# Kernel tuning notes

Hardware: AMD Instinct MI355X
Metric: run time of the kernel (lower is better)

## Reference

```python
import jax, jax.numpy as jnp
import numpy as np

B, T, E = 2, 2048, 1024
H = 16
D = E // H  # 64

def setup_inputs() -> dict:
    key = jax.random.key(0)
    kx, kq, kk, kv, ko = jax.random.split(key, 5)
    s = 1.0 / np.sqrt(E)
    return {
        "x":  jax.random.normal(kx, (B, T, E), dtype=jnp.float32),
        "Wq": jax.random.normal(kq, (E, E), dtype=jnp.float32) * s,
        "Wk": jax.random.normal(kk, (E, E), dtype=jnp.float32) * s,
        "Wv": jax.random.normal(kv, (E, E), dtype=jnp.float32) * s,
        "Wo": jax.random.normal(ko, (E, E), dtype=jnp.float32) * s,
    }

def reference(x, Wq, Wk, Wv, Wo):
    # Faithful to the torch module, including its quirks:
    #  - head split is a raw .view(B, H, T, D) reshape (NOT a transpose split)
    #  - masked_fill result is discarded in the original, so NO causal mask is applied
    #  - dropout = 0.0 -> identity
    b, t, e = x.shape
    q = jnp.reshape(x @ Wq, (b, H, t, D))
    k = jnp.reshape(x @ Wk, (b, H, t, D))
    v = jnp.reshape(x @ Wv, (b, H, t, D))
    # raw_score = q @ k^T ; softmax over keys of raw_score / sqrt(head_dim)
    scores = jnp.einsum("bhtd,bhsd->bhts", q, k) / jnp.sqrt(jnp.asarray(D, x.dtype))
    attn = jax.nn.softmax(scores, axis=-1)
    h = jnp.einsum("bhts,bhsd->bhtd", attn, v)           # (B,H,T,D)
    h = jnp.reshape(h, (b, t, e))                         # .view(B, T, -1)
    return h @ Wo
```

## Files before the change

kernel.cpp:

```cpp
#include <hip/hip_runtime.h>
#include <hip/hip_bf16.h>
#include <math.h>

#define BB 2
#define TT 2048
#define EE 1024
#define HH 16
#define DD 64
#define MM (BB*TT)

typedef __bf16 bf16;
typedef bf16 bf16x8 __attribute__((ext_vector_type(8)));
typedef bf16 bf16x4 __attribute__((ext_vector_type(4)));
typedef float f32x4 __attribute__((ext_vector_type(4)));

#define MFMA16(a,b,c) __builtin_amdgcn_mfma_f32_16x16x32_bf16((a),(b),(c),0,0,0)

__device__ __forceinline__ void gload_lds16(const void* g, void* l) {
  __builtin_amdgcn_global_load_lds(
      (const __attribute__((address_space(1))) unsigned int*)g,
      (__attribute__((address_space(3))) unsigned int*)l, 16, 0, 0);
}

__device__ __forceinline__ unsigned short bits(bf16 h) {
  return __builtin_bit_cast(unsigned short, h);
}

__global__ __launch_bounds__(256) void prep(const float* __restrict__ x,
                                            const float* __restrict__ w0,
                                            const float* __restrict__ w1,
                                            const float* __restrict__ w2,
                                            const float* __restrict__ w3,
                                            bf16* __restrict__ xb,
                                            bf16* t0, bf16* t1, bf16* t2, bf16* t3) {
  __shared__ bf16 tile[64][65];
  const int bid = blockIdx.x;
  if (bid < 4096) {
    const int i = bid * 256 + threadIdx.x;
    float4 f = ((const float4*)x)[i];
    bf16x4 h;
    h[0] = (bf16)f.x; h[1] = (bf16)f.y; h[2] = (bf16)f.z; h[3] = (bf16)f.w;
    ((bf16x4*)xb)[i] = h;
    return;
  }
  const int t = bid - 4096;
  const int z = t >> 8, rem = t & 255;
  const float* W = z == 0 ? w0 : z == 1 ? w1 : z == 2 ? w2 : w3;
  bf16* T = z == 0 ? t0 : z == 1 ? t1 : z == 2 ? t2 : t3;
  const int n0 = (rem & 15) * 64, k0 = (rem >> 4) * 64;
#pragma unroll
  for (int i = 0; i < 16; i++) {
    int idx = threadIdx.x + i * 256;
    int r = idx >> 6, c = idx & 63;
    tile[c][r] = (bf16)W[(size_t)(k0 + r) * EE + n0 + c];
  }
  __syncthreads();
#pragma unroll
  for (int i = 0; i < 16; i++) {
    int idx = threadIdx.x + i * 256;
    int r = idx >> 6, c = idx & 63;
    T[(size_t)(n0 + r) * EE + k0 + c] = tile[r][c];
  }
}

template <typename OutT>
__device__ __forceinline__ void gemm_core(const bf16* __restrict__ A, const bf16* __restrict__ Bt,
                                          OutT* __restrict__ C, bf16* As, bf16* Bs) {
  const int tid = threadIdx.x;
  const int w = tid >> 6, lane = tid & 63;
  const int lg = lane >> 4, lr = lane & 15;
  const int row0 = blockIdx.y * 128, col0 = blockIdx.x * 128;
  const int wrow = (w >> 1) * 64, wcol = (w & 1) * 64;
  f32x4 acc[4][4];
#pragma unroll
  for (int m = 0; m < 4; m++)
#pragma unroll
    for (int n = 0; n < 4; n++) acc[m][n] = f32x4{0.f, 0.f, 0.f, 0.f};

  for (int kt = 0; kt < EE; kt += 32) {
#pragma unroll
    for (int i = 0; i < 2; i++) {
      const int c = i * 4 + w;
      const int row = c * 16 + (lane >> 2);
      const int kof = (lane & 3) * 8;
      gload_lds16(A + (size_t)(row0 + row) * EE + kt + kof, &As[c * 512]);
      gload_lds16(Bt + (size_t)(col0 + row) * EE + kt + kof, &Bs[c * 512]);
    }
    __syncthreads();
    bf16x8 a[4], b[4];
#pragma unroll
    for (int m = 0; m < 4; m++)
      a[m] = *(const bf16x8*)&As[(wrow + m * 16 + lr) * 32 + lg * 8];
#pragma unroll
    for (int n = 0; n < 4; n++)
      b[n] = *(const bf16x8*)&Bs[(wcol + n * 16 + lr) * 32 + lg * 8];
#pragma unroll
    for (int m = 0; m < 4; m++)
#pragma unroll
      for (int n = 0; n < 4; n++) acc[m][n] = MFMA16(a[m], b[n], acc[m][n]);
    __syncthreads();
  }
#pragma unroll
  for (int m = 0; m < 4; m++)
#pragma unroll
    for (int n = 0; n < 4; n++)
#pragma unroll
      for (int r = 0; r < 4; r++) {
        const int rr = row0 + wrow + m * 16 + lg * 4 + r;
        const int cc = col0 + wcol + n * 16 + lr;
        C[(size_t)rr * EE + cc] = (OutT)acc[m][n][r];
      }
}

__global__ __launch_bounds__(256) void gemm_qkv(const bf16* __restrict__ A,
                                                const bf16* __restrict__ w0,
                                                const bf16* __restrict__ w1,
                                                const bf16* __restrict__ w2,
                                                bf16* o0, bf16* o1, bf16* o2) {
  __shared__ __align__(16) bf16 As[128 * 32];
  __shared__ __align__(16) bf16 Bs[128 * 32];
  const bf16* Bt = (blockIdx.z == 0) ? w0 : (blockIdx.z == 1) ? w1 : w2;
  bf16* C = (blockIdx.z == 0) ? o0 : (blockIdx.z == 1) ? o1 : o2;
  gemm_core<bf16>(A, Bt, C, As, Bs);
}

__global__ __launch_bounds__(256) void gemm_out(const bf16* __restrict__ A,
                                                const bf16* __restrict__ Bt,
                                                float* __restrict__ C) {
  __shared__ __align__(16) bf16 As[128 * 32];
  __shared__ __align__(16) bf16 Bs[64 * 32];
  const int tid = threadIdx.x;
  const int w = tid >> 6, lane = tid & 63;
  const int lg = lane >> 4, lr = lane & 15;
  const int row0 = blockIdx.y * 128, col0 = blockIdx.x * 64;
  const int wrow = (w >> 1) * 64, wcol = (w & 1) * 32;
  f32x4 acc[4][2];
#pragma unroll
  for (int m = 0; m < 4; m++)
#pragma unroll
    for (int n = 0; n < 2; n++) acc[m][n] = f32x4{0.f, 0.f, 0.f, 0.f};

  for (int kt = 0; kt < EE; kt += 32) {
#pragma unroll
    for (int i = 0; i < 3; i++) {
      const int c = i * 4 + w;
      const int r16 = lane >> 2, kof = (lane & 3) * 8;
      if (c < 8)
        gload_lds16(A + (size_t)(row0 + c * 16 + r16) * EE + kt + kof, &As[c * 512]);
      else
        gload_lds16(Bt + (size_t)(col0 + (c - 8) * 16 + r16) * EE + kt + kof,
                    &Bs[(c - 8) * 512]);
    }
    __syncthreads();
    bf16x8 a[4], b[2];
#pragma unroll
    for (int m = 0; m < 4; m++)
      a[m] = *(const bf16x8*)&As[(wrow + m * 16 + lr) * 32 + lg * 8];
#pragma unroll
    for (int n = 0; n < 2; n++)
      b[n] = *(const bf16x8*)&Bs[(wcol + n * 16 + lr) * 32 + lg * 8];
#pragma unroll
    for (int m = 0; m < 4; m++)
#pragma unroll
      for (int n = 0; n < 2; n++) acc[m][n] = MFMA16(a[m], b[n], acc[m][n]);
    __syncthreads();
  }
#pragma unroll
  for (int m = 0; m < 4; m++)
#pragma unroll
    for (int n = 0; n < 2; n++)
#pragma unroll
      for (int r = 0; r < 4; r++) {
        const int rr = row0 + wrow + m * 16 + lg * 4 + r;
        const int cc = col0 + wcol + n * 16 + lr;
        C[(size_t)rr * EE + cc] = acc[m][n][r];
      }
}

__global__ __launch_bounds__(256, 2) void flash_attn(const bf16* __restrict__ Q,
                                                     const bf16* __restrict__ K,
                                                     const bf16* __restrict__ V,
                                                     bf16* __restrict__ Hout) {
  const int tid = threadIdx.x;
  const int w = tid >> 6, lane = tid & 63;
  const int hi = lane >> 4, lr = lane & 15;
  const int qh = w & 1, sh2 = w >> 1;

  const int bid = blockIdx.x + 16 * blockIdx.y;
  const int sid = (bid & 7) * 64 + (bid >> 3);
  const int qb = sid & 15, bh = sid >> 4;

  const size_t base = (size_t)(bh >> 4) * TT * EE + (size_t)(bh & 15) * 128 * EE;
  const bf16* qh_p = Q + base;
  const bf16* kh = K + base;
  const bf16* vh = V + base;
  bf16* hh = Hout + base;
  const int qbase = qb * 128 + qh * 64;

  __shared__ __align__(16) bf16 smem[4 * 64 * 72];
  bf16* KsBuf = smem;
  bf16* VtBuf = smem + 2 * 64 * 72;

  const float qscale = 0.18033688011112042f;
  bf16x8 aq[4][2];
#pragma unroll
  for (int rg = 0; rg < 4; rg++)
#pragma unroll
    for (int kk = 0; kk < 2; kk++) {
      bf16x8 qv = *(const bf16x8*)(qh_p + (size_t)(qbase + rg * 16 + lr) * DD + kk * 32 + hi * 8);
#pragma unroll
      for (int j = 0; j < 8; j++) qv[j] = (bf16)(qscale * (float)qv[j]);
      aq[rg][kk] = qv;
    }

  float l_[4] = {0.f, 0.f, 0.f, 0.f};
  f32x4 o[4][4];
#pragma unroll
  for (int rg = 0; rg < 4; rg++)
#pragma unroll
    for (int d = 0; d < 4; d++) o[rg][d] = f32x4{0.f, 0.f, 0.f, 0.f};

  const int krow = tid >> 2, kg8 = (tid & 3) * 8;
  const int vsp = tid & 31, vdb = (tid >> 5) * 4;
  const int s0p = 2 * vsp;
  const int vcs = (s0p & 32) | (((s0p >> 2) & 3) << 3) | (((s0p >> 4) & 1) << 2) | (s0p & 3);

  bf16x8 kr0 = *(const bf16x8*)(kh + (size_t)krow * DD + kg8);
  bf16x8 kr1 = *(const bf16x8*)(kh + (size_t)krow * DD + kg8 + 32);
  bf16x4 va0 = *(const bf16x4*)(vh + (size_t)(2 * vsp) * DD + vdb);
  bf16x4 vb0 = *(const bf16x4*)(vh + (size_t)(2 * vsp + 1) * DD + vdb);
  bf16x4 va1 = *(const bf16x4*)(vh + (size_t)(2 * vsp) * DD + vdb + 32);
  bf16x4 vb1 = *(const bf16x4*)(vh + (size_t)(2 * vsp + 1) * DD + vdb + 32);
  *(bf16x8*)&KsBuf[krow * 72 + kg8] = kr0;
  *(bf16x8*)&KsBuf[krow * 72 + kg8 + 32] = kr1;
#pragma unroll
  for (int j = 0; j < 4; j++) {
    unsigned u0 = (unsigned)bits(va0[j]) | ((unsigned)bits(vb0[j]) << 16);
    unsigned u1 = (unsigned)bits(va1[j]) | ((unsigned)bits(vb1[j]) << 16);
    *(unsigned*)&VtBuf[(vdb + j) * 72 + vcs] = u0;
    *(unsigned*)&VtBuf[(vdb + 32 + j) * 72 + vcs] = u1;
  }
  kr0 = *(const bf16x8*)(kh + (size_t)(64 + krow) * DD + kg8);
  kr1 = *(const bf16x8*)(kh + (size_t)(64 + krow) * DD + kg8 + 32);
  va0 = *(const bf16x4*)(vh + (size_t)(64 + 2 * vsp) * DD + vdb);
  vb0 = *(const bf16x4*)(vh + (size_t)(64 + 2 * vsp + 1) * DD + vdb);
  va1 = *(const bf16x4*)(vh + (size_t)(64 + 2 * vsp) * DD + vdb + 32);
  vb1 = *(const bf16x4*)(vh + (size_t)(64 + 2 * vsp + 1) * DD + vdb + 32);
  __syncthreads();

  for (int t = 0; t < TT / 64; t++) {
    const bf16* Kc = &KsBuf[(t & 1) * 64 * 72];
    const bf16* Vc = &VtBuf[(t & 1) * 64 * 72];

    f32x4 sA[4][2];
#pragma unroll
    for (int rg = 0; rg < 4; rg++)
#pragma unroll
      for (int cfl = 0; cfl < 2; cfl++) sA[rg][cfl] = f32x4{0.f, 0.f, 0.f, 0.f};
#pragma unroll
    for (int cfl = 0; cfl < 2; cfl++)
#pragma unroll
      for (int kk = 0; kk < 2; kk++) {
        bf16x8 bk = *(const bf16x8*)&Kc[(sh2 * 32 + cfl * 16 + lr) * 72 + kk * 32 + hi * 8];
#pragma unroll
        for (int rg = 0; rg < 4; rg++) sA[rg][cfl] = MFMA16(bk, aq[rg][kk], sA[rg][cfl]);
      }

    bf16x8 bp[4];
#pragma unroll
    for (int rg = 0; rg < 4; rg++) {
      f32x4 pr[2];
#pragma unroll
      for (int cfl = 0; cfl < 2; cfl++)
#pragma unroll
        for (int r = 0; r < 4; r++) {
          float p = __builtin_amdgcn_exp2f(sA[rg][cfl][r]);
          l_[rg] += p;
          pr[cfl][r] = p;
        }
#pragma unroll
      for (int j = 0; j < 8; j++) bp[rg][j] = (bf16)pr[j >> 2][j & 3];
    }

#pragma unroll
    for (int dblk = 0; dblk < 4; dblk++) {
      bf16x8 av = *(const bf16x8*)&Vc[(dblk * 16 + lr) * 72 + sh2 * 32 + hi * 8];
#pragma unroll
      for (int rg = 0; rg < 4; rg++) o[rg][dblk] = MFMA16(av, bp[rg], o[rg][dblk]);
    }

    if (t < TT / 64 - 1) {
      bf16* Kn = &KsBuf[((t + 1) & 1) * 64 * 72];
      bf16* Vn = &VtBuf[((t + 1) & 1) * 64 * 72];
      *(bf16x8*)&Kn[krow * 72 + kg8] = kr0;
      *(bf16x8*)&Kn[krow * 72 + kg8 + 32] = kr1;
#pragma unroll
      for (int j = 0; j < 4; j++) {
        unsigned u0 = (unsigned)bits(va0[j]) | ((unsigned)bits(vb0[j]) << 16);
        unsigned u1 = (unsigned)bits(va1[j]) | ((unsigned)bits(vb1[j]) << 16);
        *(unsigned*)&Vn[(vdb + j) * 72 + vcs] = u0;
        *(unsigned*)&Vn[(vdb + 32 + j) * 72 + vcs] = u1;
      }
      if (t < TT / 64 - 2) {
        const int s2 = (t + 2) * 64;
        kr0 = *(const bf16x8*)(kh + (size_t)(s2 + krow) * DD + kg8);
        kr1 = *(const bf16x8*)(kh + (size_t)(s2 + krow) * DD + kg8 + 32);
        va0 = *(const bf16x4*)(vh + (size_t)(s2 + 2 * vsp) * DD + vdb);
        vb0 = *(const bf16x4*)(vh + (size_t)(s2 + 2 * vsp + 1) * DD + vdb);
        va1 = *(const bf16x4*)(vh + (size_t)(s2 + 2 * vsp) * DD + vdb + 32);
        vb1 = *(const bf16x4*)(vh + (size_t)(s2 + 2 * vsp + 1) * DD + vdb + 32);
      }
    }
    __syncthreads();
  }

  float lt[4];
#pragma unroll
  for (int rg = 0; rg < 4; rg++) {
    lt[rg] = l_[rg];
    lt[rg] += __shfl_xor(lt[rg], 16);
    lt[rg] += __shfl_xor(lt[rg], 32);
  }
  float* sc = (float*)smem;
  float* scl = sc + 2 * 64 * 68;
  if (sh2 == 1) {
#pragma unroll
    for (int rg = 0; rg < 4; rg++) {
#pragma unroll
      for (int dblk = 0; dblk < 4; dblk++)
        *(f32x4*)&sc[qh * 4352 + (rg * 16 + lr) * 68 + dblk * 16 + 4 * hi] = o[rg][dblk];
      if (hi == 0) scl[qh * 64 + rg * 16 + lr] = lt[rg];
    }
  }
  __syncthreads();
  if (sh2 == 0) {
#pragma unroll
    for (int rg = 0; rg < 4; rg++) {
      const float ltot = lt[rg] + scl[qh * 64 + rg * 16 + lr];
      const float inv = 1.0f / ltot;
#pragma unroll
      for (int dblk = 0; dblk < 4; dblk++) {
        f32x4 ob = *(const f32x4*)&sc[qh * 4352 + (rg * 16 + lr) * 68 + dblk * 16 + 4 * hi];
        bf16x4 st;
#pragma unroll
        for (int r = 0; r < 4; r++) st[r] = (bf16)((o[rg][dblk][r] + ob[r]) * inv);
        *(bf16x4*)(hh + (size_t)(qbase + rg * 16 + lr) * DD + dblk * 16 + 4 * hi) = st;
      }
    }
  }
}

extern "C" void kernel_launch(void* const* d_in, const int* in_sizes, int n_in,
                              void* d_out, int out_size, void* d_ws, size_t ws_size,
                              hipStream_t stream) {
  const float* x  = (const float*)d_in[0];
  const float* Wq = (const float*)d_in[1];
  const float* Wk = (const float*)d_in[2];
  const float* Wv = (const float*)d_in[3];
  const float* Wo = (const float*)d_in[4];
  float* out = (float*)d_out;

  bf16* xb  = (bf16*)d_ws;
  bf16* wqt = xb + (size_t)MM * EE;
  bf16* wkt = wqt + (size_t)EE * EE;
  bf16* wvt = wkt + (size_t)EE * EE;
  bf16* wot = wvt + (size_t)EE * EE;
  bf16* Qb  = wot + (size_t)EE * EE;
  bf16* Kb  = Qb + (size_t)MM * EE;
  bf16* Vb  = Kb + (size_t)MM * EE;
  bf16* Hb  = xb;

  prep<<<dim3(5120), 256, 0, stream>>>(x, Wq, Wk, Wv, Wo, xb, wqt, wkt, wvt, wot);
  gemm_qkv<<<dim3(8, 32, 3), 256, 0, stream>>>(xb, wqt, wkt, wvt, Qb, Kb, Vb);
  flash_attn<<<dim3(16, 32), 256, 0, stream>>>(Qb, Kb, Vb, Hb);
  gemm_out<<<dim3(16, 32), 256, 0, stream>>>(Hb, wot, out);
}
```

Before: 114.7 us.

## Software-pipeline QK^T one tile ahead in flash attention and reuse gemm_core for output projection

The attention loop now computes the QK^T scores for tile t+1 before doing the exp and PV products for tile t. K is staged two tiles ahead and V one tile ahead, with the loop unrolled by two and alternating between score register sets. This is meant to overlap MFMA score work with the exp/softmax VALU work and the LDS writes. Separately, the output GEMM now calls the shared 128x128 gemm_core with a float output, halving its grid. The change adds register pressure from the doubled score accumulators, and the reworked buffer indexing is easy to get wrong.

Result: no change. 116.6 us (+1.6%).

```diff
diff --git a/kernel.cpp b/kernel.cpp
--- a/kernel.cpp
+++ b/kernel.cpp
@@ -128,53 +128,8 @@
                                                 const bf16* __restrict__ Bt,
                                                 float* __restrict__ C) {
   __shared__ __align__(16) bf16 As[128 * 32];
-  __shared__ __align__(16) bf16 Bs[64 * 32];
-  const int tid = threadIdx.x;
-  const int w = tid >> 6, lane = tid & 63;
-  const int lg = lane >> 4, lr = lane & 15;
-  const int row0 = blockIdx.y * 128, col0 = blockIdx.x * 64;
-  const int wrow = (w >> 1) * 64, wcol = (w & 1) * 32;
-  f32x4 acc[4][2];
-#pragma unroll
-  for (int m = 0; m < 4; m++)
-#pragma unroll
-    for (int n = 0; n < 2; n++) acc[m][n] = f32x4{0.f, 0.f, 0.f, 0.f};
-
-  for (int kt = 0; kt < EE; kt += 32) {
-#pragma unroll
-    for (int i = 0; i < 3; i++) {
-      const int c = i * 4 + w;
-      const int r16 = lane >> 2, kof = (lane & 3) * 8;
-      if (c < 8)
-        gload_lds16(A + (size_t)(row0 + c * 16 + r16) * EE + kt + kof, &As[c * 512]);
-      else
-        gload_lds16(Bt + (size_t)(col0 + (c - 8) * 16 + r16) * EE + kt + kof,
-                    &Bs[(c - 8) * 512]);
-    }
-    __syncthreads();
-    bf16x8 a[4], b[2];
-#pragma unroll
-    for (int m = 0; m < 4; m++)
-      a[m] = *(const bf16x8*)&As[(wrow + m * 16 + lr) * 32 + lg * 8];
-#pragma unroll
-    for (int n = 0; n < 2; n++)
-      b[n] = *(const bf16x8*)&Bs[(wcol + n * 16 + lr) * 32 + lg * 8];
-#pragma unroll
-    for (int m = 0; m < 4; m++)
-#pragma unroll
-      for (int n = 0; n < 2; n++) acc[m][n] = MFMA16(a[m], b[n], acc[m][n]);
-    __syncthreads();
-  }
-#pragma unroll
-  for (int m = 0; m < 4; m++)
-#pragma unroll
-    for (int n = 0; n < 2; n++)
-#pragma unroll
-      for (int r = 0; r < 4; r++) {
-        const int rr = row0 + wrow + m * 16 + lg * 4 + r;
-        const int cc = col0 + wcol + n * 16 + lr;
-        C[(size_t)rr * EE + cc] = acc[m][n][r];
-      }
+  __shared__ __align__(16) bf16 Bs[128 * 32];
+  gemm_core<float>(A, Bt, C, As, Bs);
 }
 
 __global__ __launch_bounds__(256, 2) void flash_attn(const bf16* __restrict__ Q,
@@ -185,6 +140,7 @@
   const int w = tid >> 6, lane = tid & 63;
   const int hi = lane >> 4, lr = lane & 15;
   const int qh = w & 1, sh2 = w >> 1;
+  const int NT = TT / 64;
 
   const int bid = blockIdx.x + 16 * blockIdx.y;
   const int sid = (bid & 7) * 64 + (bid >> 3);
@@ -225,14 +181,21 @@
   const int s0p = 2 * vsp;
   const int vcs = (s0p & 32) | (((s0p >> 2) & 3) << 3) | (((s0p >> 4) & 1) << 2) | (s0p & 3);
 
-  bf16x8 kr0 = *(const bf16x8*)(kh + (size_t)krow * DD + kg8);
-  bf16x8 kr1 = *(const bf16x8*)(kh + (size_t)krow * DD + kg8 + 32);
-  bf16x4 va0 = *(const bf16x4*)(vh + (size_t)(2 * vsp) * DD + vdb);
-  bf16x4 vb0 = *(const bf16x4*)(vh + (size_t)(2 * vsp + 1) * DD + vdb);
-  bf16x4 va1 = *(const bf16x4*)(vh + (size_t)(2 * vsp) * DD + vdb + 32);
-  bf16x4 vb1 = *(const bf16x4*)(vh + (size_t)(2 * vsp + 1) * DD + vdb + 32);
+  bf16x8 kr0, kr1;
+  bf16x4 va0, vb0, va1, vb1;
+
+  kr0 = *(const bf16x8*)(kh + (size_t)krow * DD + kg8);
+  kr1 = *(const bf16x8*)(kh + (size_t)krow * DD + kg8 + 32);
   *(bf16x8*)&KsBuf[krow * 72 + kg8] = kr0;
   *(bf16x8*)&KsBuf[krow * 72 + kg8 + 32] = kr1;
+  kr0 = *(const bf16x8*)(kh + (size_t)(64 + krow) * DD + kg8);
+  kr1 = *(const bf16x8*)(kh + (size_t)(64 + krow) * DD + kg8 + 32);
+  *(bf16x8*)&KsBuf[64 * 72 + krow * 72 + kg8] = kr0;
+  *(bf16x8*)&KsBuf[64 * 72 + krow * 72 + kg8 + 32] = kr1;
+  va0 = *(const bf16x4*)(vh + (size_t)(2 * vsp) * DD + vdb);
+  vb0 = *(const bf16x4*)(vh + (size_t)(2 * vsp + 1) * DD + vdb);
+  va1 = *(const bf16x4*)(vh + (size_t)(2 * vsp) * DD + vdb + 32);
+  vb1 = *(const bf16x4*)(vh + (size_t)(2 * vsp + 1) * DD + vdb + 32);
 #pragma unroll
   for (int j = 0; j < 4; j++) {
     unsigned u0 = (unsigned)bits(va0[j]) | ((unsigned)bits(vb0[j]) << 16);
@@ -240,79 +203,102 @@
     *(unsigned*)&VtBuf[(vdb + j) * 72 + vcs] = u0;
     *(unsigned*)&VtBuf[(vdb + 32 + j) * 72 + vcs] = u1;
   }
-  kr0 = *(const bf16x8*)(kh + (size_t)(64 + krow) * DD + kg8);
-  kr1 = *(const bf16x8*)(kh + (size_t)(64 + krow) * DD + kg8 + 32);
+  kr0 = *(const bf16x8*)(kh + (size_t)(128 + krow) * DD + kg8);
+  kr1 = *(const bf16x8*)(kh + (size_t)(128 + krow) * DD + kg8 + 32);
   va0 = *(const bf16x4*)(vh + (size_t)(64 + 2 * vsp) * DD + vdb);
   vb0 = *(const bf16x4*)(vh + (size_t)(64 + 2 * vsp + 1) * DD + vdb);
   va1 = *(const bf16x4*)(vh + (size_t)(64 + 2 * vsp) * DD + vdb + 32);
   vb1 = *(const bf16x4*)(vh + (size_t)(64 + 2 * vsp + 1) * DD + vdb + 32);
   __syncthreads();
 
-  for (int t = 0; t < TT / 64; t++) {
-    const bf16* Kc = &KsBuf[(t & 1) * 64 * 72];
-    const bf16* Vc = &VtBuf[(t & 1) * 64 * 72];
-
-    f32x4 sA[4][2];
-#pragma unroll
-    for (int rg = 0; rg < 4; rg++)
-#pragma unroll
-      for (int cfl = 0; cfl < 2; cfl++) sA[rg][cfl] = f32x4{0.f, 0.f, 0.f, 0.f};
-#pragma unroll
-    for (int cfl = 0; cfl < 2; cfl++)
-#pragma unroll
-      for (int kk = 0; kk < 2; kk++) {
-        bf16x8 bk = *(const bf16x8*)&Kc[(sh2 * 32 + cfl * 16 + lr) * 72 + kk * 32 + hi * 8];
-#pragma unroll
-        for (int rg = 0; rg < 4; rg++) sA[rg][cfl] = MFMA16(bk, aq[rg][kk], sA[rg][cfl]);
-      }
-
-    bf16x8 bp[4];
-#pragma unroll
-    for (int rg = 0; rg < 4; rg++) {
-      f32x4 pr[2];
-#pragma unroll
-      for (int cfl = 0; cfl < 2; cfl++)
-#pragma unroll
-        for (int r = 0; r < 4; r++) {
-          float p = __builtin_amdgcn_exp2f(sA[rg][cfl][r]);
-          l_[rg] += p;
-          pr[cfl][r] = p;
-        }
-#pragma unroll
-      for (int j = 0; j < 8; j++) bp[rg][j] = (bf16)pr[j >> 2][j & 3];
-    }
-
-#pragma unroll
-    for (int dblk = 0; dblk < 4; dblk++) {
-      bf16x8 av = *(const bf16x8*)&Vc[(dblk * 16 + lr) * 72 + sh2 * 32 + hi * 8];
-#pragma unroll
-      for (int rg = 0; rg < 4; rg++) o[rg][dblk] = MFMA16(av, bp[rg], o[rg][dblk]);
-    }
-
-    if (t < TT / 64 - 1) {
-      bf16* Kn = &KsBuf[((t + 1) & 1) * 64 * 72];
-      bf16* Vn = &VtBuf[((t + 1) & 1) * 64 * 72];
-      *(bf16x8*)&Kn[krow * 72 + kg8] = kr0;
-      *(bf16x8*)&Kn[krow * 72 + kg8 + 32] = kr1;
-#pragma unroll
-      for (int j = 0; j < 4; j++) {
-        unsigned u0 = (unsigned)bits(va0[j]) | ((unsigned)bits(vb0[j]) << 16);
-        unsigned u1 = (unsigned)bits(va1[j]) | ((unsigned)bits(vb1[j]) << 16);
-        *(unsigned*)&Vn[(vdb + j) * 72 + vcs] = u0;
-        *(unsigned*)&Vn[(vdb + 32 + j) * 72 + vcs] = u1;
-      }
-      if (t < TT / 64 - 2) {
-        const int s2 = (t + 2) * 64;
-        kr0 = *(const bf16x8*)(kh + (size_t)(s2 + krow) * DD + kg8);
-        kr1 = *(const bf16x8*)(kh + (size_t)(s2 + krow) * DD + kg8 + 32);
-        va0 = *(const bf16x4*)(vh + (size_t)(s2 + 2 * vsp) * DD + vdb);
-        vb0 = *(const bf16x4*)(vh + (size_t)(s2 + 2 * vsp + 1) * DD + vdb);
-        va1 = *(const bf16x4*)(vh + (size_t)(s2 + 2 * vsp) * DD + vdb + 32);
-        vb1 = *(const bf16x4*)(vh + (size_t)(s2 + 2 * vsp + 1) * DD + vdb + 32);
-      }
-    }
-    __syncthreads();
-  }
+  f32x4 sA_a[4][2], sA_b[4][2];
+
+#pragma unroll
+  for (int rg = 0; rg < 4; rg++)
+#pragma unroll
+    for (int cfl = 0; cfl < 2; cfl++) sA_a[rg][cfl] = f32x4{0.f, 0.f, 0.f, 0.f};
+#pragma unroll
+  for (int cfl = 0; cfl < 2; cfl++)
+#pragma unroll
+    for (int kk = 0; kk < 2; kk++) {
+      bf16x8 bk = *(const bf16x8*)&KsBuf[(sh2 * 32 + cfl * 16 + lr) * 72 + kk * 32 + hi * 8];
+#pragma unroll
+      for (int rg = 0; rg < 4; rg++) sA_a[rg][cfl] = MFMA16(bk, aq[rg][kk], sA_a[rg][cfl]);
+    }
+  __syncthreads();
+
+#define FLASH_ITER(SCUR, SNEXT, T)                                                     \
+  {                                                                                    \
+                       \
+    if ((T) + 1 < NT) {                                                                \
+      const bf16* Kn_ = &KsBuf[(((T) + 1) & 1) * 64 * 72];                             \
+      _Pragma("unroll") for (int rg = 0; rg < 4; rg++)                                 \
+        _Pragma("unroll") for (int cfl = 0; cfl < 2; cfl++)                            \
+          SNEXT[rg][cfl] = f32x4{0.f, 0.f, 0.f, 0.f};                                  \
+      _Pragma("unroll") for (int cfl = 0; cfl < 2; cfl++)                              \
+        _Pragma("unroll") for (int kk = 0; kk < 2; kk++) {                             \
+          bf16x8 bk = *(const bf16x8*)&Kn_[(sh2 * 32 + cfl * 16 + lr) * 72 +           \
+                                           kk * 32 + hi * 8];                          \
+          _Pragma("unroll") for (int rg = 0; rg < 4; rg++)                             \
+            SNEXT[rg][cfl] = MFMA16(bk, aq[rg][kk], SNEXT[rg][cfl]);                   \
+        }                                                                              \
+    }                                                                                  \
+                        \
+    bf16x8 bp[4];                                                                      \
+    _Pragma("unroll") for (int rg = 0; rg < 4; rg++) {                                 \
+      f32x4 pr[2];                                                                     \
+      _Pragma("unroll") for (int cfl = 0; cfl < 2; cfl++)                              \
+        _Pragma("unroll") for (int r = 0; r < 4; r++) {                                \
+          float p = __builtin_amdgcn_exp2f(SCUR[rg][cfl][r]);                          \
+          l_[rg] += p;                                                                 \
+          pr[cfl][r] = p;                                                              \
+        }                                                                              \
+      _Pragma("unroll") for (int j = 0; j < 8; j++) bp[rg][j] = (bf16)pr[j >> 2][j & 3]; \
+    }                                                                                  \
+                                                         \
+    {                                                                                  \
+      const bf16* Vc_ = &VtBuf[((T) & 1) * 64 * 72];                                   \
+      _Pragma("unroll") for (int dblk = 0; dblk < 4; dblk++) {                         \
+        bf16x8 av = *(const bf16x8*)&Vc_[(dblk * 16 + lr) * 72 + sh2 * 32 + hi * 8];   \
+        _Pragma("unroll") for (int rg = 0; rg < 4; rg++)                               \
+          o[rg][dblk] = MFMA16(av, bp[rg], o[rg][dblk]);                               \
+      }                                                                                \
+    }                                                                                  \
+             \
+    if ((T) + 2 < NT) {                                                                \
+      bf16* Kw_ = &KsBuf[((T) & 1) * 64 * 72];                                         \
+      *(bf16x8*)&Kw_[krow * 72 + kg8] = kr0;                                           \
+      *(bf16x8*)&Kw_[krow * 72 + kg8 + 32] = kr1;                                      \
+      if ((T) + 3 < NT) {                                                              \
+        const int s3 = ((T) + 3) * 64;                                                 \
+        kr0 = *(const bf16x8*)(kh + (size_t)(s3 + krow) * DD + kg8);                   \
+        kr1 = *(const bf16x8*)(kh + (size_t)(s3 + krow) * DD + kg8 + 32);              \
+      }                                                                                \
+    }                                                                                  \
+    if ((T) + 1 < NT) {                                                                \
+      bf16* Vw_ = &VtBuf[(((T) + 1) & 1) * 64 * 72];                                   \
+      _Pragma("unroll") for (int j = 0; j < 4; j++) {                                  \
+        unsigned u0 = (unsigned)bits(va0[j]) | ((unsigned)bits(vb0[j]) << 16);         \
+        unsigned u1 = (unsigned)bits(va1[j]) | ((unsigned)bits(vb1[j]) << 16);         \
+        *(unsigned*)&Vw_[(vdb + j) * 72 + vcs] = u0;                                   \
+        *(unsigned*)&Vw_[(vdb + 32 + j) * 72 + vcs] = u1;                              \
+      }                                                                                \
+      if ((T) + 2 < NT) {                                                              \
+        const int s2 = ((T) + 2) * 64;                                                 \
+        va0 = *(const bf16x4*)(vh + (size_t)(s2 + 2 * vsp) * DD + vdb);                \
+        vb0 = *(const bf16x4*)(vh + (size_t)(s2 + 2 * vsp + 1) * DD + vdb);            \
+        va1 = *(const bf16x4*)(vh + (size_t)(s2 + 2 * vsp) * DD + vdb + 32);           \
+        vb1 = *(const bf16x4*)(vh + (size_t)(s2 + 2 * vsp + 1) * DD + vdb + 32);       \
+      }                                                                                \
+    }                                                                                  \
+    __syncthreads();                                                                   \
+  }
+
+  for (int t = 0; t < NT; t += 2) {
+    FLASH_ITER(sA_a, sA_b, t);
+    FLASH_ITER(sA_b, sA_a, t + 1);
+  }
+#undef FLASH_ITER
 
   float lt[4];
 #pragma unroll
@@ -373,5 +359,5 @@
   prep<<<dim3(5120), 256, 0, stream>>>(x, Wq, Wk, Wv, Wo, xb, wqt, wkt, wvt, wot);
   gemm_qkv<<<dim3(8, 32, 3), 256, 0, stream>>>(xb, wqt, wkt, wvt, Qb, Kb, Vb);
   flash_attn<<<dim3(16, 32), 256, 0, stream>>>(Qb, Kb, Vb, Hb);
-  gemm_out<<<dim3(16, 32), 256, 0, stream>>>(Hb, wot, out);
-}
+  gemm_out<<<dim3(8, 32), 256, 0, stream>>>(Hb, wot, out);
+}
```

## Process 128-key tiles per sync in flash attention and reuse gemm_core for output GEMM

Applied to the files above, without the earlier changes.

The attention loop now stages 128 keys (two 64-key halves) of K and transposed V per shared-memory buffer, which halves the number of barriers and register-prefetch rounds. This doubles LDS usage and prefetch registers, which may lower occupancy. The output projection now calls the shared 128x128 gemm_core template with float output, so it launches half as many blocks with larger tiles.

After: 116.9 us. No clear change (+1.9%).

```diff
diff --git a/kernel.cpp b/kernel.cpp
--- a/kernel.cpp
+++ b/kernel.cpp
@@ -128,53 +128,8 @@
                                                 const bf16* __restrict__ Bt,
                                                 float* __restrict__ C) {
   __shared__ __align__(16) bf16 As[128 * 32];
-  __shared__ __align__(16) bf16 Bs[64 * 32];
-  const int tid = threadIdx.x;
-  const int w = tid >> 6, lane = tid & 63;
-  const int lg = lane >> 4, lr = lane & 15;
-  const int row0 = blockIdx.y * 128, col0 = blockIdx.x * 64;
-  const int wrow = (w >> 1) * 64, wcol = (w & 1) * 32;
-  f32x4 acc[4][2];
-#pragma unroll
-  for (int m = 0; m < 4; m++)
-#pragma unroll
-    for (int n = 0; n < 2; n++) acc[m][n] = f32x4{0.f, 0.f, 0.f, 0.f};
-
-  for (int kt = 0; kt < EE; kt += 32) {
-#pragma unroll
-    for (int i = 0; i < 3; i++) {
-      const int c = i * 4 + w;
-      const int r16 = lane >> 2, kof = (lane & 3) * 8;
-      if (c < 8)
-        gload_lds16(A + (size_t)(row0 + c * 16 + r16) * EE + kt + kof, &As[c * 512]);
-      else
-        gload_lds16(Bt + (size_t)(col0 + (c - 8) * 16 + r16) * EE + kt + kof,
-                    &Bs[(c - 8) * 512]);
-    }
-    __syncthreads();
-    bf16x8 a[4], b[2];
-#pragma unroll
-    for (int m = 0; m < 4; m++)
-      a[m] = *(const bf16x8*)&As[(wrow + m * 16 + lr) * 32 + lg * 8];
-#pragma unroll
-    for (int n = 0; n < 2; n++)
-      b[n] = *(const bf16x8*)&Bs[(wcol + n * 16 + lr) * 32 + lg * 8];
-#pragma unroll
-    for (int m = 0; m < 4; m++)
-#pragma unroll
-      for (int n = 0; n < 2; n++) acc[m][n] = MFMA16(a[m], b[n], acc[m][n]);
-    __syncthreads();
-  }
-#pragma unroll
-  for (int m = 0; m < 4; m++)
-#pragma unroll
-    for (int n = 0; n < 2; n++)
-#pragma unroll
-      for (int r = 0; r < 4; r++) {
-        const int rr = row0 + wrow + m * 16 + lg * 4 + r;
-        const int cc = col0 + wcol + n * 16 + lr;
-        C[(size_t)rr * EE + cc] = acc[m][n][r];
-      }
+  __shared__ __align__(16) bf16 Bs[128 * 32];
+  gemm_core<float>(A, Bt, C, As, Bs);
 }
 
 __global__ __launch_bounds__(256, 2) void flash_attn(const bf16* __restrict__ Q,
@@ -185,6 +140,7 @@
   const int w = tid >> 6, lane = tid & 63;
   const int hi = lane >> 4, lr = lane & 15;
   const int qh = w & 1, sh2 = w >> 1;
+  const int NTP = TT / 128;
 
   const int bid = blockIdx.x + 16 * blockIdx.y;
   const int sid = (bid & 7) * 64 + (bid >> 3);
@@ -197,9 +153,9 @@
   bf16* hh = Hout + base;
   const int qbase = qb * 128 + qh * 64;
 
-  __shared__ __align__(16) bf16 smem[4 * 64 * 72];
+  __shared__ __align__(16) bf16 smem[2 * 128 * 72 + 2 * 64 * 136];
   bf16* KsBuf = smem;
-  bf16* VtBuf = smem + 2 * 64 * 72;
+  bf16* VtBuf = smem + 2 * 128 * 72;
 
   const float qscale = 0.18033688011112042f;
   bf16x8 aq[4][2];
@@ -225,94 +181,103 @@
   const int s0p = 2 * vsp;
   const int vcs = (s0p & 32) | (((s0p >> 2) & 3) << 3) | (((s0p >> 4) & 1) << 2) | (s0p & 3);
 
-  bf16x8 kr0 = *(const bf16x8*)(kh + (size_t)krow * DD + kg8);
-  bf16x8 kr1 = *(const bf16x8*)(kh + (size_t)krow * DD + kg8 + 32);
-  bf16x4 va0 = *(const bf16x4*)(vh + (size_t)(2 * vsp) * DD + vdb);
-  bf16x4 vb0 = *(const bf16x4*)(vh + (size_t)(2 * vsp + 1) * DD + vdb);
-  bf16x4 va1 = *(const bf16x4*)(vh + (size_t)(2 * vsp) * DD + vdb + 32);
-  bf16x4 vb1 = *(const bf16x4*)(vh + (size_t)(2 * vsp + 1) * DD + vdb + 32);
-  *(bf16x8*)&KsBuf[krow * 72 + kg8] = kr0;
-  *(bf16x8*)&KsBuf[krow * 72 + kg8 + 32] = kr1;
-#pragma unroll
-  for (int j = 0; j < 4; j++) {
-    unsigned u0 = (unsigned)bits(va0[j]) | ((unsigned)bits(vb0[j]) << 16);
-    unsigned u1 = (unsigned)bits(va1[j]) | ((unsigned)bits(vb1[j]) << 16);
-    *(unsigned*)&VtBuf[(vdb + j) * 72 + vcs] = u0;
-    *(unsigned*)&VtBuf[(vdb + 32 + j) * 72 + vcs] = u1;
-  }
-  kr0 = *(const bf16x8*)(kh + (size_t)(64 + krow) * DD + kg8);
-  kr1 = *(const bf16x8*)(kh + (size_t)(64 + krow) * DD + kg8 + 32);
-  va0 = *(const bf16x4*)(vh + (size_t)(64 + 2 * vsp) * DD + vdb);
-  vb0 = *(const bf16x4*)(vh + (size_t)(64 + 2 * vsp + 1) * DD + vdb);
-  va1 = *(const bf16x4*)(vh + (size_t)(64 + 2 * vsp) * DD + vdb + 32);
-  vb1 = *(const bf16x4*)(vh + (size_t)(64 + 2 * vsp + 1) * DD + vdb + 32);
+  bf16x8 kr0, kr1, kr2, kr3;
+  bf16x4 va0, vb0, va1, vb1, va2, vb2, va3, vb3;
+
+#define LOAD_PAIR_REGS(S0)                                                        \
+  {                                                                               \
+    kr0 = *(const bf16x8*)(kh + (size_t)((S0) + krow) * DD + kg8);                \
+    kr1 = *(const bf16x8*)(kh + (size_t)((S0) + krow) * DD + kg8 + 32);           \
+    kr2 = *(const bf16x8*)(kh + (size_t)((S0) + 64 + krow) * DD + kg8);           \
+    kr3 = *(const bf16x8*)(kh + (size_t)((S0) + 64 + krow) * DD + kg8 + 32);      \
+    va0 = *(const bf16x4*)(vh + (size_t)((S0) + 2 * vsp) * DD + vdb);             \
+    vb0 = *(const bf16x4*)(vh + (size_t)((S0) + 2 * vsp + 1) * DD + vdb);         \
+    va1 = *(const bf16x4*)(vh + (size_t)((S0) + 2 * vsp) * DD + vdb + 32);        \
+    vb1 = *(const bf16x4*)(vh + (size_t)((S0) + 2 * vsp + 1) * DD + vdb + 32);    \
+    va2 = *(const bf16x4*)(vh + (size_t)((S0) + 64 + 2 * vsp) * DD + vdb);        \
+    vb2 = *(const bf16x4*)(vh + (size_t)((S0) + 64 + 2 * vsp + 1) * DD + vdb);    \
+    va3 = *(const bf16x4*)(vh + (size_t)((S0) + 64 + 2 * vsp) * DD + vdb + 32);   \
+    vb3 = *(const bf16x4*)(vh + (size_t)((S0) + 64 + 2 * vsp + 1) * DD + vdb + 32); \
+  }
+
+#define STORE_PAIR(KB, VB)                                                        \
+  {                                                                               \
+    *(bf16x8*)&(KB)[krow * 72 + kg8] = kr0;                                       \
+    *(bf16x8*)&(KB)[krow * 72 + kg8 + 32] = kr1;                                  \
+    *(bf16x8*)&(KB)[(64 + krow) * 72 + kg8] = kr2;                                \
+    *(bf16x8*)&(KB)[(64 + krow) * 72 + kg8 + 32] = kr3;                           \
+    _Pragma("unroll") for (int j = 0; j < 4; j++) {                               \
+      unsigned u0 = (unsigned)bits(va0[j]) | ((unsigned)bits(vb0[j]) << 16);      \
+      unsigned u1 = (unsigned)bits(va1[j]) | ((unsigned)bits(vb1[j]) << 16);      \
+      unsigned u2 = (unsigned)bits(va2[j]) | ((unsigned)bits(vb2[j]) << 16);      \
+      unsigned u3 = (unsigned)bits(va3[j]) | ((unsigned)bits(vb3[j]) << 16);      \
+      *(unsigned*)&(VB)[(vdb + j) * 136 + vcs] = u0;                              \
+      *(unsigned*)&(VB)[(vdb + 32 + j) * 136 + vcs] = u1;                         \
+      *(unsigned*)&(VB)[(vdb + j) * 136 + 64 + vcs] = u2;                         \
+      *(unsigned*)&(VB)[(vdb + 32 + j) * 136 + 64 + vcs] = u3;                    \
+    }                                                                             \
+  }
+
+  LOAD_PAIR_REGS(0);
+  STORE_PAIR(KsBuf, VtBuf);
+  LOAD_PAIR_REGS(128);
   __syncthreads();
 
-  for (int t = 0; t < TT / 64; t++) {
-    const bf16* Kc = &KsBuf[(t & 1) * 64 * 72];
-    const bf16* Vc = &VtBuf[(t & 1) * 64 * 72];
-
-    f32x4 sA[4][2];
-#pragma unroll
-    for (int rg = 0; rg < 4; rg++)
-#pragma unroll
-      for (int cfl = 0; cfl < 2; cfl++) sA[rg][cfl] = f32x4{0.f, 0.f, 0.f, 0.f};
-#pragma unroll
-    for (int cfl = 0; cfl < 2; cfl++)
-#pragma unroll
-      for (int kk = 0; kk < 2; kk++) {
-        bf16x8 bk = *(const bf16x8*)&Kc[(sh2 * 32 + cfl * 16 + lr) * 72 + kk * 32 + hi * 8];
-#pragma unroll
-        for (int rg = 0; rg < 4; rg++) sA[rg][cfl] = MFMA16(bk, aq[rg][kk], sA[rg][cfl]);
+  for (int tp = 0; tp < NTP; tp++) {
+    const bf16* Kc = &KsBuf[(tp & 1) * 128 * 72];
+    const bf16* Vc = &VtBuf[(tp & 1) * 64 * 136];
+
+#pragma unroll
+    for (int th = 0; th < 2; th++) {
+      f32x4 sA[4][2];
+#pragma unroll
+      for (int rg = 0; rg < 4; rg++)
+#pragma unroll
+        for (int cfl = 0; cfl < 2; cfl++) sA[rg][cfl] = f32x4{0.f, 0.f, 0.f, 0.f};
+#pragma unroll
+      for (int cfl = 0; cfl < 2; cfl++)
+#pragma unroll
+        for (int kk = 0; kk < 2; kk++) {
+          bf16x8 bk = *(const bf16x8*)&Kc[(th * 64 + sh2 * 32 + cfl * 16 + lr) * 72 +
+                                          kk * 32 + hi * 8];
+#pragma unroll
+          for (int rg = 0; rg < 4; rg++) sA[rg][cfl] = MFMA16(bk, aq[rg][kk], sA[rg][cfl]);
+        }
+
+      bf16x8 bp[4];
+#pragma unroll
+      for (int rg = 0; rg < 4; rg++) {
+        f32x4 pr[2];
+#pragma unroll
+        for (int cfl = 0; cfl < 2; cfl++)
+#pragma unroll
+          for (int r = 0; r < 4; r++) {
+            float p = __builtin_amdgcn_exp2f(sA[rg][cfl][r]);
+            l_[rg] += p;
+            pr[cfl][r] = p;
+          }
+#pragma unroll
+        for (int j = 0; j < 8; j++) bp[rg][j] = (bf16)pr[j >> 2][j & 3];
       }
 
-    bf16x8 bp[4];
-#pragma unroll
-    for (int rg = 0; rg < 4; rg++) {
-      f32x4 pr[2];
-#pragma unroll
-      for (int cfl = 0; cfl < 2; cfl++)
-#pragma unroll
-        for (int r = 0; r < 4; r++) {
-          float p = __builtin_amdgcn_exp2f(sA[rg][cfl][r]);
-          l_[rg] += p;
-          pr[cfl][r] = p;
-        }
-#pragma unroll
-      for (int j = 0; j < 8; j++) bp[rg][j] = (bf16)pr[j >> 2][j & 3];
-    }
-
-#pragma unroll
-    for (int dblk = 0; dblk < 4; dblk++) {
-      bf16x8 av = *(const bf16x8*)&Vc[(dblk * 16 + lr) * 72 + sh2 * 32 + hi * 8];
-#pragma unroll
-      for (int rg = 0; rg < 4; rg++) o[rg][dblk] = MFMA16(av, bp[rg], o[rg][dblk]);
-    }
-
-    if (t < TT / 64 - 1) {
-      bf16* Kn = &KsBuf[((t + 1) & 1) * 64 * 72];
-      bf16* Vn = &VtBuf[((t + 1) & 1) * 64 * 72];
-      *(bf16x8*)&Kn[krow * 72 + kg8] = kr0;
-      *(bf16x8*)&Kn[krow * 72 + kg8 + 32] = kr1;
-#pragma unroll
-      for (int j = 0; j < 4; j++) {
-        unsigned u0 = (unsigned)bits(va0[j]) | ((unsigned)bits(vb0[j]) << 16);
-        unsigned u1 = (unsigned)bits(va1[j]) | ((unsigned)bits(vb1[j]) << 16);
-        *(unsigned*)&Vn[(vdb + j) * 72 + vcs] = u0;
-        *(unsigned*)&Vn[(vdb + 32 + j) * 72 + vcs] = u1;
+#pragma unroll
+      for (int dblk = 0; dblk < 4; dblk++) {
+        bf16x8 av = *(const bf16x8*)&Vc[(dblk * 16 + lr) * 136 + th * 64 + sh2 * 32 + hi * 8];
+#pragma unroll
+        for (int rg = 0; rg < 4; rg++) o[rg][dblk] = MFMA16(av, bp[rg], o[rg][dblk]);
       }
-      if (t < TT / 64 - 2) {
-        const int s2 = (t + 2) * 64;
-        kr0 = *(const bf16x8*)(kh + (size_t)(s2 + krow) * DD + kg8);
-        kr1 = *(const bf16x8*)(kh + (size_t)(s2 + krow) * DD + kg8 + 32);
-        va0 = *(const bf16x4*)(vh + (size_t)(s2 + 2 * vsp) * DD + vdb);
-        vb0 = *(const bf16x4*)(vh + (size_t)(s2 + 2 * vsp + 1) * DD + vdb);
-        va1 = *(const bf16x4*)(vh + (size_t)(s2 + 2 * vsp) * DD + vdb + 32);
-        vb1 = *(const bf16x4*)(vh + (size_t)(s2 + 2 * vsp + 1) * DD + vdb + 32);
-      }
+    }
+
+    if (tp < NTP - 1) {
+      bf16* Kn = &KsBuf[((tp + 1) & 1) * 128 * 72];
+      bf16* Vn = &VtBuf[((tp + 1) & 1) * 64 * 136];
+      STORE_PAIR(Kn, Vn);
+      if (tp < NTP - 2) LOAD_PAIR_REGS((tp + 2) * 128);
     }
     __syncthreads();
   }
+#undef LOAD_PAIR_REGS
+#undef STORE_PAIR
 
   float lt[4];
 #pragma unroll
@@ -373,5 +338,5 @@
   prep<<<dim3(5120), 256, 0, stream>>>(x, Wq, Wk, Wv, Wo, xb, wqt, wkt, wvt, wot);
   gemm_qkv<<<dim3(8, 32, 3), 256, 0, stream>>>(xb, wqt, wkt, wvt, Qb, Kb, Vb);
   flash_attn<<<dim3(16, 32), 256, 0, stream>>>(Qb, Kb, Vb, Hb);
-  gemm_out<<<dim3(16, 32), 256, 0, stream>>>(Hb, wot, out);
-}
+  gemm_out<<<dim3(8, 32), 256, 0, stream>>>(Hb, wot, out);
+}
```

## Fuse x fp32-to-bf16 conversion into QKV GEMM and enlarge output GEMM tiles

Applied to the files above, without the earlier changes.

Drops the separate conversion of x to bf16 in the prep kernel. The QKV GEMM now loads fp32 x directly, converts it in registers and writes it to LDS, which removes one round trip of the activation through global memory. Both GEMMs also get a swizzled block-to-tile mapping meant to improve L2 reuse, and the output GEMM moves from 128x64 to 128x128 tiles. The cost is that the A operand now loads synchronously instead of going through the async global-to-LDS path, x is re-read as fp32 (twice the bytes) by every column tile, and the output GEMM launches fewer blocks.

Result: no change. 113.7 us, median of 2 (-0.8%).

```diff
diff --git a/kernel.cpp b/kernel.cpp
--- a/kernel.cpp
+++ b/kernel.cpp
@@ -26,24 +26,13 @@
   return __builtin_bit_cast(unsigned short, h);
 }
 
-__global__ __launch_bounds__(256) void prep(const float* __restrict__ x,
-                                            const float* __restrict__ w0,
+__global__ __launch_bounds__(256) void prep(const float* __restrict__ w0,
                                             const float* __restrict__ w1,
                                             const float* __restrict__ w2,
                                             const float* __restrict__ w3,
-                                            bf16* __restrict__ xb,
                                             bf16* t0, bf16* t1, bf16* t2, bf16* t3) {
   __shared__ bf16 tile[64][65];
-  const int bid = blockIdx.x;
-  if (bid < 4096) {
-    const int i = bid * 256 + threadIdx.x;
-    float4 f = ((const float4*)x)[i];
-    bf16x4 h;
-    h[0] = (bf16)f.x; h[1] = (bf16)f.y; h[2] = (bf16)f.z; h[3] = (bf16)f.w;
-    ((bf16x4*)xb)[i] = h;
-    return;
-  }
-  const int t = bid - 4096;
+  const int t = blockIdx.x;
   const int z = t >> 8, rem = t & 255;
   const float* W = z == 0 ? w0 : z == 1 ? w1 : z == 2 ? w2 : w3;
   bf16* T = z == 0 ? t0 : z == 1 ? t1 : z == 2 ? t2 : t3;
@@ -63,56 +52,7 @@
   }
 }
 
-template <typename OutT>
-__device__ __forceinline__ void gemm_core(const bf16* __restrict__ A, const bf16* __restrict__ Bt,
-                                          OutT* __restrict__ C, bf16* As, bf16* Bs) {
-  const int tid = threadIdx.x;
-  const int w = tid >> 6, lane = tid & 63;
-  const int lg = lane >> 4, lr = lane & 15;
-  const int row0 = blockIdx.y * 128, col0 = blockIdx.x * 128;
-  const int wrow = (w >> 1) * 64, wcol = (w & 1) * 64;
-  f32x4 acc[4][4];
-#pragma unroll
-  for (int m = 0; m < 4; m++)
-#pragma unroll
-    for (int n = 0; n < 4; n++) acc[m][n] = f32x4{0.f, 0.f, 0.f, 0.f};
-
-  for (int kt = 0; kt < EE; kt += 32) {
-#pragma unroll
-    for (int i = 0; i < 2; i++) {
-      const int c = i * 4 + w;
-      const int row = c * 16 + (lane >> 2);
-      const int kof = (lane & 3) * 8;
-      gload_lds16(A + (size_t)(row0 + row) * EE + kt + kof, &As[c * 512]);
-      gload_lds16(Bt + (size_t)(col0 + row) * EE + kt + kof, &Bs[c * 512]);
-    }
-    __syncthreads();
-    bf16x8 a[4], b[4];
-#pragma unroll
-    for (int m = 0; m < 4; m++)
-      a[m] = *(const bf16x8*)&As[(wrow + m * 16 + lr) * 32 + lg * 8];
-#pragma unroll
-    for (int n = 0; n < 4; n++)
-      b[n] = *(const bf16x8*)&Bs[(wcol + n * 16 + lr) * 32 + lg * 8];
-#pragma unroll
-    for (int m = 0; m < 4; m++)
-#pragma unroll
-      for (int n = 0; n < 4; n++) acc[m][n] = MFMA16(a[m], b[n], acc[m][n]);
-    __syncthreads();
-  }
-#pragma unroll
-  for (int m = 0; m < 4; m++)
-#pragma unroll
-    for (int n = 0; n < 4; n++)
-#pragma unroll
-      for (int r = 0; r < 4; r++) {
-        const int rr = row0 + wrow + m * 16 + lg * 4 + r;
-        const int cc = col0 + wcol + n * 16 + lr;
-        C[(size_t)rr * EE + cc] = (OutT)acc[m][n][r];
-      }
-}
-
-__global__ __launch_bounds__(256) void gemm_qkv(const bf16* __restrict__ A,
+__global__ __launch_bounds__(256) void gemm_qkv(const float* __restrict__ X,
                                                 const bf16* __restrict__ w0,
                                                 const bf16* __restrict__ w1,
                                                 const bf16* __restrict__ w2,
@@ -121,54 +61,109 @@
   __shared__ __align__(16) bf16 Bs[128 * 32];
   const bf16* Bt = (blockIdx.z == 0) ? w0 : (blockIdx.z == 1) ? w1 : w2;
   bf16* C = (blockIdx.z == 0) ? o0 : (blockIdx.z == 1) ? o1 : o2;
-  gemm_core<bf16>(A, Bt, C, As, Bs);
+  const int bid = blockIdx.x + 8 * blockIdx.y;
+  const int sid = (bid & 7) * 32 + (bid >> 3);
+  const int rowt = sid & 31, colt = sid >> 5;
+  const int row0 = rowt * 128, col0 = colt * 128;
+
+  const int tid = threadIdx.x;
+  const int w = tid >> 6, lane = tid & 63;
+  const int lg = lane >> 4, lr = lane & 15;
+  const int wrow = (w >> 1) * 64, wcol = (w & 1) * 64;
+  const int arow = lane >> 2, akof = (lane & 3) * 8;
+  f32x4 acc[4][4];
+#pragma unroll
+  for (int m = 0; m < 4; m++)
+#pragma unroll
+    for (int n = 0; n < 4; n++) acc[m][n] = f32x4{0.f, 0.f, 0.f, 0.f};
+
+  for (int kt = 0; kt < EE; kt += 32) {
+#pragma unroll
+    for (int i = 0; i < 2; i++) {
+      const int c = i * 4 + w;
+      const int row = c * 16 + arow;
+      gload_lds16(Bt + (size_t)(col0 + row) * EE + kt + akof, &Bs[c * 512]);
+      const float* src = X + (size_t)(row0 + row) * EE + kt + akof;
+      f32x4 f0 = *(const f32x4*)src;
+      f32x4 f1 = *(const f32x4*)(src + 4);
+      bf16x8 v;
+#pragma unroll
+      for (int j = 0; j < 4; j++) { v[j] = (bf16)f0[j]; v[4 + j] = (bf16)f1[j]; }
+      *(bf16x8*)&As[c * 512 + lane * 8] = v;
+    }
+    __syncthreads();
+    bf16x8 a[4], b[4];
+#pragma unroll
+    for (int m = 0; m < 4; m++)
+      a[m] = *(const bf16x8*)&As[(wrow + m * 16 + lr) * 32 + lg * 8];
+#pragma unroll
+    for (int n = 0; n < 4; n++)
+      b[n] = *(const bf16x8*)&Bs[(wcol + n * 16 + lr) * 32 + lg * 8];
+#pragma unroll
+    for (int m = 0; m < 4; m++)
+#pragma unroll
+      for (int n = 0; n < 4; n++) acc[m][n] = MFMA16(a[m], b[n], acc[m][n]);
+    __syncthreads();
+  }
+#pragma unroll
+  for (int m = 0; m < 4; m++)
+#pragma unroll
+    for (int n = 0; n < 4; n++)
+#pragma unroll
+      for (int r = 0; r < 4; r++) {
+        const int rr = row0 + wrow + m * 16 + lg * 4 + r;
+        const int cc = col0 + wcol + n * 16 + lr;
+        C[(size_t)rr * EE + cc] = (bf16)acc[m][n][r];
+      }
 }
 
 __global__ __launch_bounds__(256) void gemm_out(const bf16* __restrict__ A,
                                                 const bf16* __restrict__ Bt,
                                                 float* __restrict__ C) {
   __shared__ __align__(16) bf16 As[128 * 32];
-  __shared__ __align__(16) bf16 Bs[64 * 32];
+  __shared__ __align__(16) bf16 Bs[128 * 32];
+  const int bid = blockIdx.x + 8 * blockIdx.y;
+  const int sid = (bid & 7) * 32 + (bid >> 3);
+  const int rowt = sid & 31, colt = sid >> 5;
+  const int row0 = rowt * 128, col0 = colt * 128;
+
   const int tid = threadIdx.x;
   const int w = tid >> 6, lane = tid & 63;
   const int lg = lane >> 4, lr = lane & 15;
-  const int row0 = blockIdx.y * 128, col0 = blockIdx.x * 64;
-  const int wrow = (w >> 1) * 64, wcol = (w & 1) * 32;
-  f32x4 acc[4][2];
+  const int wrow = (w >> 1) * 64, wcol = (w & 1) * 64;
+  f32x4 acc[4][4];
 #pragma unroll
   for (int m = 0; m < 4; m++)
 #pragma unroll
-    for (int n = 0; n < 2; n++) acc[m][n] = f32x4{0.f, 0.f, 0.f, 0.f};
+    for (int n = 0; n < 4; n++) acc[m][n] = f32x4{0.f, 0.f, 0.f, 0.f};
 
   for (int kt = 0; kt < EE; kt += 32) {
 #pragma unroll
-    for (int i = 0; i < 3; i++) {
+    for (int i = 0; i < 2; i++) {
       const int c = i * 4 + w;
-      const int r16 = lane >> 2, kof = (lane & 3) * 8;
-      if (c < 8)
-        gload_lds16(A + (size_t)(row0 + c * 16 + r16) * EE + kt + kof, &As[c * 512]);
-      else
-        gload_lds16(Bt + (size_t)(col0 + (c - 8) * 16 + r16) * EE + kt + kof,
-                    &Bs[(c - 8) * 512]);
-    }
-    __syncthreads();
-    bf16x8 a[4], b[2];
+      const int row = c * 16 + (lane >> 2);
+      const int kof = (lane & 3) * 8;
+      gload_lds16(A + (size_t)(row0 + row) * EE + kt + kof, &As[c * 512]);
+      gload_lds16(Bt + (size_t)(col0 + row) * EE + kt + kof, &Bs[c * 512]);
+    }
+    __syncthreads();
+    bf16x8 a[4], b[4];
 #pragma unroll
     for (int m = 0; m < 4; m++)
       a[m] = *(const bf16x8*)&As[(wrow + m * 16 + lr) * 32 + lg * 8];
 #pragma unroll
-    for (int n = 0; n < 2; n++)
+    for (int n = 0; n < 4; n++)
       b[n] = *(const bf16x8*)&Bs[(wcol + n * 16 + lr) * 32 + lg * 8];
 #pragma unroll
     for (int m = 0; m < 4; m++)
 #pragma unroll
-      for (int n = 0; n < 2; n++) acc[m][n] = MFMA16(a[m], b[n], acc[m][n]);
+      for (int n = 0; n < 4; n++) acc[m][n] = MFMA16(a[m], b[n], acc[m][n]);
     __syncthreads();
   }
 #pragma unroll
   for (int m = 0; m < 4; m++)
 #pragma unroll
-    for (int n = 0; n < 2; n++)
+    for (int n = 0; n < 4; n++)
 #pragma unroll
       for (int r = 0; r < 4; r++) {
         const int rr = row0 + wrow + m * 16 + lg * 4 + r;
@@ -360,18 +355,17 @@
   const float* Wo = (const float*)d_in[4];
   float* out = (float*)d_out;
 
-  bf16* xb  = (bf16*)d_ws;
-  bf16* wqt = xb + (size_t)MM * EE;
+  bf16* Hb  = (bf16*)d_ws;
+  bf16* wqt = Hb + (size_t)MM * EE;
   bf16* wkt = wqt + (size_t)EE * EE;
   bf16* wvt = wkt + (size_t)EE * EE;
   bf16* wot = wvt + (size_t)EE * EE;
   bf16* Qb  = wot + (size_t)EE * EE;
   bf16* Kb  = Qb + (size_t)MM * EE;
   bf16* Vb  = Kb + (size_t)MM * EE;
-  bf16* Hb  = xb;
-
-  prep<<<dim3(5120), 256, 0, stream>>>(x, Wq, Wk, Wv, Wo, xb, wqt, wkt, wvt, wot);
-  gemm_qkv<<<dim3(8, 32, 3), 256, 0, stream>>>(xb, wqt, wkt, wvt, Qb, Kb, Vb);
+
+  prep<<<dim3(1024), 256, 0, stream>>>(Wq, Wk, Wv, Wo, wqt, wkt, wvt, wot);
+  gemm_qkv<<<dim3(8, 32, 3), 256, 0, stream>>>(x, wqt, wkt, wvt, Qb, Kb, Vb);
   flash_attn<<<dim3(16, 32), 256, 0, stream>>>(Qb, Kb, Vb, Hb);
-  gemm_out<<<dim3(16, 32), 256, 0, stream>>>(Hb, wot, out);
-}
+  gemm_out<<<dim3(8, 32), 256, 0, stream>>>(Hb, wot, out);
+}
```
